# Optimization experiments

Hardware: AMD Instinct MI355X
Metric: run time of the kernel (lower is better)

## Reference

```python
import jax, jax.numpy as jnp
import numpy as np


def _rnn_layer(x, W_ih, W_hh, b_ih, b_hh):
    """PyTorch tanh RNN layer, batch_first. x: [B,T,I] -> out: [B,T,H].
    h_t = tanh(x_t @ W_ih.T + b_ih + h_{t-1} @ W_hh.T + b_hh), h_0 = 0.
    """
    B = x.shape[0]
    H = W_hh.shape[0]
    # precompute input contribution for all timesteps at once: [T,B,H]
    pre = jnp.einsum('bti,hi->tbh', x, W_ih) + b_ih + b_hh

    def step(h, pre_t):
        h_new = jnp.tanh(pre_t + h @ W_hh.T)
        return h_new, h_new

    h0 = jnp.zeros((B, H), dtype=x.dtype)
    _, out = jax.lax.scan(step, h0, pre)  # out: [T,B,H]
    return jnp.transpose(out, (1, 0, 2))  # [B,T,H]


def setup_inputs() -> dict:
    key = jax.random.key(0)
    ks = jax.random.split(key, 11)
    B, T, I, H = 2048, 512, 8, 64
    s_i = 1.0 / np.sqrt(H)
    return {
        'x': jax.random.normal(ks[0], (B, T, I), dtype=jnp.float32),
        'W_ih0': jax.random.normal(ks[1], (H, I), dtype=jnp.float32) * s_i,
        'W_hh0': jax.random.normal(ks[2], (H, H), dtype=jnp.float32) * s_i,
        'b_ih0': jax.random.normal(ks[3], (H,), dtype=jnp.float32) * s_i,
        'b_hh0': jax.random.normal(ks[4], (H,), dtype=jnp.float32) * s_i,
        'W_ih1': jax.random.normal(ks[5], (H, H), dtype=jnp.float32) * s_i,
        'W_hh1': jax.random.normal(ks[6], (H, H), dtype=jnp.float32) * s_i,
        'b_ih1': jax.random.normal(ks[7], (H,), dtype=jnp.float32) * s_i,
        'b_hh1': jax.random.normal(ks[8], (H,), dtype=jnp.float32) * s_i,
        'fc_w': jax.random.normal(ks[9], (1, H), dtype=jnp.float32) * s_i,
        'fc_b': jax.random.normal(ks[10], (1,), dtype=jnp.float32) * s_i,
    }


def reference(x, W_ih0, W_hh0, b_ih0, b_hh0, W_ih1, W_hh1, b_ih1, b_hh1, fc_w, fc_b):
    out0 = _rnn_layer(x, W_ih0, W_hh0, b_ih0, b_hh0)     # [B,T,H]
    out1 = _rnn_layer(out0, W_ih1, W_hh1, b_ih1, b_hh1)  # [B,T,H]
    last = out1[:, -1, :]                                # [B,H]
    return last @ fc_w.T + fc_b                          # [B,1]
```

## Files before the change

kernel.cpp:

```cpp
#include <hip/hip_runtime.h>

#define T_STEPS 512
#define BATCH   2048
#define HID     64
#define IN0     8
#define SPW     16
#define NBLK    (BATCH / SPW)
#define SS      8
#define NSS     (T_STEPS / SS)

#define KSC 2.885390081777927f

typedef _Float16 h2 __attribute__((ext_vector_type(2)));
typedef _Float16 h8 __attribute__((ext_vector_type(8)));
typedef float    f4 __attribute__((ext_vector_type(4)));

#define MFMA(a, b, c) __builtin_amdgcn_mfma_f32_16x16x32_f16((a), (b), (c), 0, 0, 0)

union F8 { h8 v; h2 p[4]; };

__device__ __forceinline__ h2 pkrtz(float a, float b) {
    return __builtin_bit_cast(h2, __builtin_amdgcn_cvt_pkrtz(a, b));
}

__device__ __forceinline__ float tanh_pre(float kx) {
    float e = __builtin_amdgcn_exp2f(kx);
    return 1.0f - 2.0f * __builtin_amdgcn_rcpf(e + 1.0f);
}

__device__ __forceinline__ h8 load_frag_f16_s(const float* Wrow, float s) {
    const float4* p = (const float4*)Wrow;
    float4 a = p[0], b = p[1];
    F8 f; f.p[0] = pkrtz(s * a.x, s * a.y); f.p[1] = pkrtz(s * a.z, s * a.w);
          f.p[2] = pkrtz(s * b.x, s * b.y); f.p[3] = pkrtz(s * b.z, s * b.w);
    return f.v;
}

#define LDS_BARRIER() asm volatile("s_waitcnt lgkmcnt(0)\n\ts_barrier" ::: "memory")

__global__ __launch_bounds__(256, 1)
void rnn2_k4(const float* __restrict__ x,
             const float* __restrict__ Wih0, const float* __restrict__ Whh0,
             const float* __restrict__ bih0, const float* __restrict__ bhh0,
             const float* __restrict__ Wih1, const float* __restrict__ Whh1,
             const float* __restrict__ bih1, const float* __restrict__ bhh1,
             const float* __restrict__ fcw,  const float* __restrict__ fcb,
             float* __restrict__ out) {
    const int tid  = threadIdx.x;
    const int w    = tid >> 6;
    const int lane = tid & 63;
    const int n    = lane & 15;
    const int q    = lane >> 4;
    const int bseq = blockIdx.x * SPW;
    const bool isL0 = (w < 2);
    const int hf   = isL0 ? w : (w - 2);
    const int mt0  = 2 * hf;

    __shared__ __align__(16) h8 X0[2][2][64];
    __shared__ __align__(16) h8 X1[2][2][64];
    __shared__ float red[2][SPW];

    {
        h8 z = {};
        X0[w >> 1][w & 1][lane] = z;
        X1[w >> 1][w & 1][lane] = z;
    }
    __syncthreads();

    const h2 z2 = pkrtz(0.f, 0.f);
    const float fcb0 = fcb[0];

    if (isL0) {
        h8 wh[2][2], wi[2];
        f4 bias[2];
        #pragma unroll
        for (int l = 0; l < 2; ++l) {
            const int mt = mt0 + l;
            const int ar = 32 * (mt >> 1) + 4 * (mt & 1) + 8 * (n >> 2) + (n & 3);
            #pragma unroll
            for (int kt = 0; kt < 2; ++kt)
                wh[l][kt] = load_frag_f16_s(Whh0 + ar * HID + 32 * kt + 8 * q, KSC);
            const float2 ww = *(const float2*)(Wih0 + ar * IN0 + 2 * q);
            F8 f; f.p[0] = pkrtz(KSC * ww.x, KSC * ww.y);
            f.p[1] = z2; f.p[2] = z2; f.p[3] = z2;
            wi[l] = f.v;
            #pragma unroll
            for (int r = 0; r < 4; ++r) {
                const int cr = 32 * (mt >> 1) + 4 * (mt & 1) + 8 * q + r;
                bias[l][r] = KSC * (bih0[cr] + bhh0[cr]);
            }
        }
        const float* xrow = x + ((size_t)(bseq + n)) * T_STEPS * IN0 + 2 * q;
        float2 xb[SS];
        #pragma unroll
        for (int i = 0; i < SS; ++i)
            xb[i] = *(const float2*)(xrow + i * IN0);

        h8 own = {};
        for (int s = 0; s < NSS; ++s) {
            #pragma unroll
            for (int i = 0; i < SS; ++i) {
                const int t = SS * s + i;
                const int bf = t & 1;
                const h8 other = X0[bf ^ 1][hf ^ 1][lane];
                F8 xf; xf.p[0] = pkrtz(xb[i].x, xb[i].y);
                xf.p[1] = z2; xf.p[2] = z2; xf.p[3] = z2;
                f4 cp0 = MFMA(wi[0], xf.v, bias[0]);
                f4 cp1 = MFMA(wi[1], xf.v, bias[1]);
                cp0 = MFMA(wh[0][hf], own, cp0);
                cp1 = MFMA(wh[1][hf], own, cp1);
                int tn = t + SS; if (tn > T_STEPS - 1) tn = T_STEPS - 1;
                xb[i] = *(const float2*)(xrow + tn * IN0);
                f4 c0 = MFMA(wh[0][hf ^ 1], other, cp0);
                f4 c1 = MFMA(wh[1][hf ^ 1], other, cp1);
                F8 pk;
                pk.p[0] = pkrtz(tanh_pre(c0[0]), tanh_pre(c0[1]));
                pk.p[1] = pkrtz(tanh_pre(c0[2]), tanh_pre(c0[3]));
                pk.p[2] = pkrtz(tanh_pre(c1[0]), tanh_pre(c1[1]));
                pk.p[3] = pkrtz(tanh_pre(c1[2]), tanh_pre(c1[3]));
                own = pk.v;
                X0[bf][hf][lane] = own;
                LDS_BARRIER();
            }
        }
    } else {
        h8 wa[2][2], wb[2][2];
        f4 bias[2], fcv[2];
        #pragma unroll
        for (int l = 0; l < 2; ++l) {
            const int mt = mt0 + l;
            const int ar = 32 * (mt >> 1) + 4 * (mt & 1) + 8 * (n >> 2) + (n & 3);
            #pragma unroll
            for (int kt = 0; kt < 2; ++kt) {
                wa[l][kt] = load_frag_f16_s(Wih1 + ar * HID + 32 * kt + 8 * q, KSC);
                wb[l][kt] = load_frag_f16_s(Whh1 + ar * HID + 32 * kt + 8 * q, KSC);
            }
            #pragma unroll
            for (int r = 0; r < 4; ++r) {
                const int cr = 32 * (mt >> 1) + 4 * (mt & 1) + 8 * q + r;
                bias[l][r] = KSC * (bih1[cr] + bhh1[cr]);
                fcv[l][r]  = fcw[cr];
            }
        }
        h8 own1 = {};
        for (int s = 0; s < NSS; ++s) {
            #pragma unroll
            for (int i = 0; i < SS; ++i) {
                const int t = SS * s + i;
                const int bf = t & 1;
                const h8 h00 = X0[bf ^ 1][0][lane];
                const h8 h01 = X0[bf ^ 1][1][lane];
                const h8 h1o = X1[bf ^ 1][hf ^ 1][lane];
                f4 e0 = MFMA(wb[0][hf], own1, bias[0]);
                f4 e1 = MFMA(wb[1][hf], own1, bias[1]);
                e0 = MFMA(wa[0][0], h00, e0);
                e1 = MFMA(wa[1][0], h00, e1);
                e0 = MFMA(wa[0][1], h01, e0);
                e1 = MFMA(wa[1][1], h01, e1);
                e0 = MFMA(wb[0][hf ^ 1], h1o, e0);
                e1 = MFMA(wb[1][hf ^ 1], h1o, e1);
                F8 pk;
                pk.p[0] = pkrtz(tanh_pre(e0[0]), tanh_pre(e0[1]));
                pk.p[1] = pkrtz(tanh_pre(e0[2]), tanh_pre(e0[3]));
                pk.p[2] = pkrtz(tanh_pre(e1[0]), tanh_pre(e1[1]));
                pk.p[3] = pkrtz(tanh_pre(e1[2]), tanh_pre(e1[3]));
                if (i == 0) {
                    if (s != 0) { own1 = pk.v; X1[bf][hf][lane] = own1; }
                } else {
                    own1 = pk.v; X1[bf][hf][lane] = own1;
                }
                LDS_BARRIER();
            }
        }
        {
            const h8 h00 = X0[1][0][lane];
            const h8 h01 = X0[1][1][lane];
            const h8 h1o = X1[1][hf ^ 1][lane];
            f4 e0 = MFMA(wb[0][hf], own1, bias[0]);
            f4 e1 = MFMA(wb[1][hf], own1, bias[1]);
            e0 = MFMA(wa[0][0], h00, e0);
            e1 = MFMA(wa[1][0], h00, e1);
            e0 = MFMA(wa[0][1], h01, e0);
            e1 = MFMA(wa[1][1], h01, e1);
            e0 = MFMA(wb[0][hf ^ 1], h1o, e0);
            e1 = MFMA(wb[1][hf ^ 1], h1o, e1);
            float sacc = 0.f;
            #pragma unroll
            for (int r = 0; r < 4; ++r) {
                sacc += fcv[0][r] * tanh_pre(e0[r]);
                sacc += fcv[1][r] * tanh_pre(e1[r]);
            }
            sacc += __shfl_xor(sacc, 16, 64);
            sacc += __shfl_xor(sacc, 32, 64);
            if (lane < 16) red[hf][n] = sacc;
        }
    }

    __syncthreads();
    if (tid < SPW)
        out[bseq + tid] = red[0][tid] + red[1][tid] + fcb0;
}

extern "C" void kernel_launch(void* const* d_in, const int* in_sizes, int n_in,
                              void* d_out, int out_size, void* d_ws, size_t ws_size,
                              hipStream_t stream) {
    const float* x    = (const float*)d_in[0];
    const float* Wih0 = (const float*)d_in[1];
    const float* Whh0 = (const float*)d_in[2];
    const float* bih0 = (const float*)d_in[3];
    const float* bhh0 = (const float*)d_in[4];
    const float* Wih1 = (const float*)d_in[5];
    const float* Whh1 = (const float*)d_in[6];
    const float* bih1 = (const float*)d_in[7];
    const float* bhh1 = (const float*)d_in[8];
    const float* fcw  = (const float*)d_in[9];
    const float* fcb  = (const float*)d_in[10];
    float* out = (float*)d_out;

    rnn2_k4<<<dim3(NBLK), dim3(256), 0, stream>>>(
        x, Wih0, Whh0, bih0, bhh0, Wih1, Whh1, bih1, bhh1, fcw, fcb, out);
}
```

Baseline: 223.9 us.

## Split each RNN layer across four waves, one 16-row tile per wave

Each block now runs 8 waves instead of 4, with 4 waves per layer, and each wave owns a single 16-row output tile instead of two. Every wave reads the full previous hidden state back from LDS as four h4 slices rather than keeping its own half in registers. This roughly halves the MFMA chain and tanh work per wave on each serial timestep, shortening the critical path. The cost is more LDS traffic and a barrier shared by 8 waves at every step.

```diff
diff --git a/kernel.cpp b/kernel.cpp
--- a/kernel.cpp
+++ b/kernel.cpp
@@ -12,12 +12,15 @@
 #define KSC 2.885390081777927f
 
 typedef _Float16 h2 __attribute__((ext_vector_type(2)));
+typedef _Float16 h4 __attribute__((ext_vector_type(4)));
 typedef _Float16 h8 __attribute__((ext_vector_type(8)));
 typedef float    f4 __attribute__((ext_vector_type(4)));
 
 #define MFMA(a, b, c) __builtin_amdgcn_mfma_f32_16x16x32_f16((a), (b), (c), 0, 0, 0)
 
-union F8 { h8 v; h2 p[4]; };
+union F8  { h8 v; h2 p[4]; };
+union H4U { h4 v; h2 p[2]; };
+union H8Q { h8 v; h4 h[2]; };
 
 __device__ __forceinline__ h2 pkrtz(float a, float b) {
     return __builtin_bit_cast(h2, __builtin_amdgcn_cvt_pkrtz(a, b));
@@ -38,8 +41,8 @@
 
 #define LDS_BARRIER() asm volatile("s_waitcnt lgkmcnt(0)\n\ts_barrier" ::: "memory")
 
-__global__ __launch_bounds__(256, 1)
-void rnn2_k4(const float* __restrict__ x,
+__global__ __launch_bounds__(512, 1)
+void rnn2_q8(const float* __restrict__ x,
              const float* __restrict__ Wih0, const float* __restrict__ Whh0,
              const float* __restrict__ bih0, const float* __restrict__ bhh0,
              const float* __restrict__ Wih1, const float* __restrict__ Whh1,
@@ -48,47 +51,40 @@
              float* __restrict__ out) {
     const int tid  = threadIdx.x;
     const int w    = tid >> 6;
+    const int mt   = w & 3;
+    const bool isL0 = (w < 4);
     const int lane = tid & 63;
     const int n    = lane & 15;
     const int q    = lane >> 4;
     const int bseq = blockIdx.x * SPW;
-    const bool isL0 = (w < 2);
-    const int hf   = isL0 ? w : (w - 2);
-    const int mt0  = 2 * hf;
 
-    __shared__ __align__(16) h8 X0[2][2][64];
-    __shared__ __align__(16) h8 X1[2][2][64];
-    __shared__ float red[2][SPW];
+    __shared__ __align__(16) h4 X0[2][4][64];
+    __shared__ __align__(16) h4 X1[2][4][64];
+    __shared__ float red[4][SPW];
 
-    {
-        h8 z = {};
-        X0[w >> 1][w & 1][lane] = z;
-        X1[w >> 1][w & 1][lane] = z;
-    }
+    { h4 z = {}; X0[w >> 2][mt][lane] = z; X1[w >> 2][mt][lane] = z; }
     __syncthreads();
 
     const h2 z2 = pkrtz(0.f, 0.f);
     const float fcb0 = fcb[0];
+    const int ar = 32 * (mt >> 1) + 4 * (mt & 1) + 8 * (n >> 2) + (n & 3);
 
     if (isL0) {
-        h8 wh[2][2], wi[2];
-        f4 bias[2];
+        h8 wh[2], wi;
+        f4 bias;
         #pragma unroll
-        for (int l = 0; l < 2; ++l) {
-            const int mt = mt0 + l;
-            const int ar = 32 * (mt >> 1) + 4 * (mt & 1) + 8 * (n >> 2) + (n & 3);
-            #pragma unroll
-            for (int kt = 0; kt < 2; ++kt)
-                wh[l][kt] = load_frag_f16_s(Whh0 + ar * HID + 32 * kt + 8 * q, KSC);
+        for (int kt = 0; kt < 2; ++kt)
+            wh[kt] = load_frag_f16_s(Whh0 + ar * HID + 32 * kt + 8 * q, KSC);
+        {
             const float2 ww = *(const float2*)(Wih0 + ar * IN0 + 2 * q);
             F8 f; f.p[0] = pkrtz(KSC * ww.x, KSC * ww.y);
             f.p[1] = z2; f.p[2] = z2; f.p[3] = z2;
-            wi[l] = f.v;
-            #pragma unroll
-            for (int r = 0; r < 4; ++r) {
-                const int cr = 32 * (mt >> 1) + 4 * (mt & 1) + 8 * q + r;
-                bias[l][r] = KSC * (bih0[cr] + bhh0[cr]);
-            }
+            wi = f.v;
+        }
+        #pragma unroll
+        for (int r = 0; r < 4; ++r) {
+            const int cr = 32 * (mt >> 1) + 4 * (mt & 1) + 8 * q + r;
+            bias[r] = KSC * (bih0[cr] + bhh0[cr]);
         }
         const float* xrow = x + ((size_t)(bseq + n)) * T_STEPS * IN0 + 2 * q;
         float2 xb[SS];
@@ -96,109 +92,89 @@
         for (int i = 0; i < SS; ++i)
             xb[i] = *(const float2*)(xrow + i * IN0);
 
-        h8 own = {};
         for (int s = 0; s < NSS; ++s) {
             #pragma unroll
             for (int i = 0; i < SS; ++i) {
                 const int t = SS * s + i;
                 const int bf = t & 1;
-                const h8 other = X0[bf ^ 1][hf ^ 1][lane];
+                H8Q f0, f1;
+                f0.h[0] = X0[bf ^ 1][0][lane]; f0.h[1] = X0[bf ^ 1][1][lane];
+                f1.h[0] = X0[bf ^ 1][2][lane]; f1.h[1] = X0[bf ^ 1][3][lane];
                 F8 xf; xf.p[0] = pkrtz(xb[i].x, xb[i].y);
                 xf.p[1] = z2; xf.p[2] = z2; xf.p[3] = z2;
-                f4 cp0 = MFMA(wi[0], xf.v, bias[0]);
-                f4 cp1 = MFMA(wi[1], xf.v, bias[1]);
-                cp0 = MFMA(wh[0][hf], own, cp0);
-                cp1 = MFMA(wh[1][hf], own, cp1);
+                f4 cp = MFMA(wi, xf.v, bias);
                 int tn = t + SS; if (tn > T_STEPS - 1) tn = T_STEPS - 1;
                 xb[i] = *(const float2*)(xrow + tn * IN0);
-                f4 c0 = MFMA(wh[0][hf ^ 1], other, cp0);
-                f4 c1 = MFMA(wh[1][hf ^ 1], other, cp1);
-                F8 pk;
-                pk.p[0] = pkrtz(tanh_pre(c0[0]), tanh_pre(c0[1]));
-                pk.p[1] = pkrtz(tanh_pre(c0[2]), tanh_pre(c0[3]));
-                pk.p[2] = pkrtz(tanh_pre(c1[0]), tanh_pre(c1[1]));
-                pk.p[3] = pkrtz(tanh_pre(c1[2]), tanh_pre(c1[3]));
-                own = pk.v;
-                X0[bf][hf][lane] = own;
+                f4 c = MFMA(wh[0], f0.v, cp);
+                c    = MFMA(wh[1], f1.v, c);
+                H4U u;
+                u.p[0] = pkrtz(tanh_pre(c[0]), tanh_pre(c[1]));
+                u.p[1] = pkrtz(tanh_pre(c[2]), tanh_pre(c[3]));
+                X0[bf][mt][lane] = u.v;
                 LDS_BARRIER();
             }
         }
     } else {
-        h8 wa[2][2], wb[2][2];
-        f4 bias[2], fcv[2];
+        h8 wa[2], wb[2];
+        f4 bias, fcv;
         #pragma unroll
-        for (int l = 0; l < 2; ++l) {
-            const int mt = mt0 + l;
-            const int ar = 32 * (mt >> 1) + 4 * (mt & 1) + 8 * (n >> 2) + (n & 3);
-            #pragma unroll
-            for (int kt = 0; kt < 2; ++kt) {
-                wa[l][kt] = load_frag_f16_s(Wih1 + ar * HID + 32 * kt + 8 * q, KSC);
-                wb[l][kt] = load_frag_f16_s(Whh1 + ar * HID + 32 * kt + 8 * q, KSC);
-            }
-            #pragma unroll
-            for (int r = 0; r < 4; ++r) {
-                const int cr = 32 * (mt >> 1) + 4 * (mt & 1) + 8 * q + r;
-                bias[l][r] = KSC * (bih1[cr] + bhh1[cr]);
-                fcv[l][r]  = fcw[cr];
-            }
+        for (int kt = 0; kt < 2; ++kt) {
+            wa[kt] = load_frag_f16_s(Wih1 + ar * HID + 32 * kt + 8 * q, KSC);
+            wb[kt] = load_frag_f16_s(Whh1 + ar * HID + 32 * kt + 8 * q, KSC);
         }
-        h8 own1 = {};
+        #pragma unroll
+        for (int r = 0; r < 4; ++r) {
+            const int cr = 32 * (mt >> 1) + 4 * (mt & 1) + 8 * q + r;
+            bias[r] = KSC * (bih1[cr] + bhh1[cr]);
+            fcv[r]  = fcw[cr];
+        }
         for (int s = 0; s < NSS; ++s) {
             #pragma unroll
             for (int i = 0; i < SS; ++i) {
                 const int t = SS * s + i;
                 const int bf = t & 1;
-                const h8 h00 = X0[bf ^ 1][0][lane];
-                const h8 h01 = X0[bf ^ 1][1][lane];
-                const h8 h1o = X1[bf ^ 1][hf ^ 1][lane];
-                f4 e0 = MFMA(wb[0][hf], own1, bias[0]);
-                f4 e1 = MFMA(wb[1][hf], own1, bias[1]);
-                e0 = MFMA(wa[0][0], h00, e0);
-                e1 = MFMA(wa[1][0], h00, e1);
-                e0 = MFMA(wa[0][1], h01, e0);
-                e1 = MFMA(wa[1][1], h01, e1);
-                e0 = MFMA(wb[0][hf ^ 1], h1o, e0);
-                e1 = MFMA(wb[1][hf ^ 1], h1o, e1);
-                F8 pk;
-                pk.p[0] = pkrtz(tanh_pre(e0[0]), tanh_pre(e0[1]));
-                pk.p[1] = pkrtz(tanh_pre(e0[2]), tanh_pre(e0[3]));
-                pk.p[2] = pkrtz(tanh_pre(e1[0]), tanh_pre(e1[1]));
-                pk.p[3] = pkrtz(tanh_pre(e1[2]), tanh_pre(e1[3]));
+                H8Q g0, g1, k0, k1;
+                g0.h[0] = X0[bf ^ 1][0][lane]; g0.h[1] = X0[bf ^ 1][1][lane];
+                g1.h[0] = X0[bf ^ 1][2][lane]; g1.h[1] = X0[bf ^ 1][3][lane];
+                k0.h[0] = X1[bf ^ 1][0][lane]; k0.h[1] = X1[bf ^ 1][1][lane];
+                k1.h[0] = X1[bf ^ 1][2][lane]; k1.h[1] = X1[bf ^ 1][3][lane];
+                f4 e = MFMA(wa[0], g0.v, bias);
+                e    = MFMA(wa[1], g1.v, e);
+                e    = MFMA(wb[0], k0.v, e);
+                e    = MFMA(wb[1], k1.v, e);
+                H4U u;
+                u.p[0] = pkrtz(tanh_pre(e[0]), tanh_pre(e[1]));
+                u.p[1] = pkrtz(tanh_pre(e[2]), tanh_pre(e[3]));
                 if (i == 0) {
-                    if (s != 0) { own1 = pk.v; X1[bf][hf][lane] = own1; }
+                    if (s != 0) X1[bf][mt][lane] = u.v;
                 } else {
-                    own1 = pk.v; X1[bf][hf][lane] = own1;
+                    X1[bf][mt][lane] = u.v;
                 }
                 LDS_BARRIER();
             }
         }
         {
-            const h8 h00 = X0[1][0][lane];
-            const h8 h01 = X0[1][1][lane];
-            const h8 h1o = X1[1][hf ^ 1][lane];
-            f4 e0 = MFMA(wb[0][hf], own1, bias[0]);
-            f4 e1 = MFMA(wb[1][hf], own1, bias[1]);
-            e0 = MFMA(wa[0][0], h00, e0);
-            e1 = MFMA(wa[1][0], h00, e1);
-            e0 = MFMA(wa[0][1], h01, e0);
-            e1 = MFMA(wa[1][1], h01, e1);
-            e0 = MFMA(wb[0][hf ^ 1], h1o, e0);
-            e1 = MFMA(wb[1][hf ^ 1], h1o, e1);
+            H8Q g0, g1, k0, k1;
+            g0.h[0] = X0[1][0][lane]; g0.h[1] = X0[1][1][lane];
+            g1.h[0] = X0[1][2][lane]; g1.h[1] = X0[1][3][lane];
+            k0.h[0] = X1[1][0][lane]; k0.h[1] = X1[1][1][lane];
+            k1.h[0] = X1[1][2][lane]; k1.h[1] = X1[1][3][lane];
+            f4 e = MFMA(wa[0], g0.v, bias);
+            e    = MFMA(wa[1], g1.v, e);
+            e    = MFMA(wb[0], k0.v, e);
+            e    = MFMA(wb[1], k1.v, e);
             float sacc = 0.f;
             #pragma unroll
-            for (int r = 0; r < 4; ++r) {
-                sacc += fcv[0][r] * tanh_pre(e0[r]);
-                sacc += fcv[1][r] * tanh_pre(e1[r]);
-            }
+            for (int r = 0; r < 4; ++r) sacc += fcv[r] * tanh_pre(e[r]);
             sacc += __shfl_xor(sacc, 16, 64);
             sacc += __shfl_xor(sacc, 32, 64);
-            if (lane < 16) red[hf][n] = sacc;
+            if (lane < 16) red[mt][n] = sacc;
         }
     }
 
     __syncthreads();
     if (tid < SPW)
-        out[bseq + tid] = red[0][tid] + red[1][tid] + fcb0;
+        out[bseq + tid] = red[0][tid] + red[1][tid] + red[2][tid] + red[3][tid] + fcb0;
 }
 
 extern "C" void kernel_launch(void* const* d_in, const int* in_sizes, int n_in,
@@ -217,6 +193,6 @@
     const float* fcb  = (const float*)d_in[10];
     float* out = (float*)d_out;
 
-    rnn2_k4<<<dim3(NBLK), dim3(256), 0, stream>>>(
+    rnn2_q8<<<dim3(NBLK), dim3(512), 0, stream>>>(
         x, Wih0, Whh0, bih0, bhh0, Wih1, Whh1, bih1, bhh1, fcw, fcb, out);
 }
```

Result: faster. 206.4 us (-7.8%).
